# Kernel optimization log

Measured on AMD Instinct MI355X. Metric: run time of the kernel, lower is better.

Reference implementation:

```python
import jax, jax.numpy as jnp
import numpy as np
from jax import lax


def setup_inputs() -> dict:
    key = jax.random.key(0)
    ks = jax.random.split(key, 8)
    B, H, W = 1, 128, 128

    def rnd(k, shape, fan_in):
        return jax.random.normal(k, shape, dtype=jnp.float32) / np.float32(np.sqrt(fan_in))

    return {
        "x": jax.random.normal(ks[0], (B, 1, H, W), dtype=jnp.float32),
        "z": jax.random.uniform(ks[1], (B, 1), dtype=jnp.float32),
        "w_conv1": rnd(ks[2], (16, 1, 9, 9), 81),
        "b_conv1": jnp.zeros((16,), jnp.float32),
        "w_conv2": rnd(ks[3], (16, 16, 5, 5), 16 * 25),
        "b_conv2": jnp.zeros((16,), jnp.float32),
        "w_fc1": rnd(ks[4], (1024, 128), 1024),
        "b_fc1": jnp.zeros((128,), jnp.float32),
        "w_pose": rnd(ks[5], (1, 16), 1),
        "b_pose": jnp.zeros((16,), jnp.float32),
        "w_fc2": rnd(ks[6], (144, 1), 144),
        "b_fc2": jnp.zeros((1,), jnp.float32),
    }


_DN = ("NCHW", "OIHW", "NCHW")  # conv dimension numbers
_P = 32  # GQ-CNN patch size


def _maxpool2(h):
    return lax.reduce_window(h, -jnp.inf, lax.max, (1, 1, 2, 2), (1, 1, 2, 2), "VALID")


def _gqcnn(patches, z_rep, w_conv1, b_conv1, w_conv2, b_conv2,
           w_fc1, b_fc1, w_pose, b_pose, w_fc2, b_fc2):
    # patches: [N,1,32,32], z_rep: [N,1] -> quality [N,1]
    h = jax.nn.relu(lax.conv_general_dilated(patches, w_conv1, (1, 1), "SAME",
                                             dimension_numbers=_DN)
                    + b_conv1[None, :, None, None])
    h = _maxpool2(h)  # [N,16,16,16]
    h = jax.nn.relu(lax.conv_general_dilated(h, w_conv2, (1, 1), "SAME",
                                             dimension_numbers=_DN)
                    + b_conv2[None, :, None, None])
    h = _maxpool2(h)  # [N,16,8,8]
    flat = h.reshape(h.shape[0], -1)  # [N,1024]
    f = jax.nn.relu(flat @ w_fc1 + b_fc1)      # [N,128]
    p = jax.nn.relu(z_rep @ w_pose + b_pose)   # [N,16]
    return jnp.concatenate([f, p], axis=1) @ w_fc2 + b_fc2  # [N,1]


def reference(x, z, w_conv1, b_conv1, w_conv2, b_conv2,
              w_fc1, b_fc1, w_pose, b_pose, w_fc2, b_fc2):
    B, _, H, W = x.shape
    Hp, Wp = H - _P, W - _P  # loop ranges in the original: range(H-32), range(W-32)
    # Batched patch extraction replaces the O(H*W) Python loop.
    pat = lax.conv_general_dilated_patches(x, (_P, _P), (1, 1), "VALID")  # [B,1024,H-31,W-31]
    pat = pat[:, :, :Hp, :Wp]
    pat = jnp.transpose(pat, (0, 2, 3, 1)).reshape(B * Hp * Wp, 1, _P, _P)
    z_rep = jnp.repeat(z, Hp * Wp, axis=0)  # matches [B,Hp,Wp] flattening order
    q = _gqcnn(pat, z_rep, w_conv1, b_conv1, w_conv2, b_conv2,
               w_fc1, b_fc1, w_pose, b_pose, w_fc2, b_fc2)  # [N,1]
    half = _P // 2
    heat = jnp.zeros_like(x).at[:, :, half:H - half, half:W - half].set(
        q.reshape(B, 1, Hp, Wp))
    return heat
```

## Files before the change

kernel.cpp:

```cpp
#include <hip/hip_runtime.h>

typedef __attribute__((ext_vector_type(8))) short short8;
typedef __attribute__((ext_vector_type(4))) float f32x4;
typedef unsigned short u16;

__device__ __forceinline__ u16 f2bf(float f) {
    unsigned u = __builtin_bit_cast(unsigned, f);
    unsigned r = u + 0x7fffu + ((u >> 16) & 1u);
    return (u16)(r >> 16);
}

__global__ __launch_bounds__(256) void k0_prep(
    const float* __restrict__ z, const float* __restrict__ w1,
    const float* __restrict__ w2, const float* __restrict__ wfc1,
    const float* __restrict__ wpose, const float* __restrict__ bpose,
    const float* __restrict__ wfc2, const float* __restrict__ bfc2,
    float* __restrict__ out, u16* __restrict__ w1p, u16* __restrict__ w2p,
    u16* __restrict__ fc1T, float* __restrict__ cst)
{
    int gt = blockIdx.x * 256 + threadIdx.x;
    out[gt] = 0.f;

    if (gt < 2560) {
        int l = (gt >> 3) & 63, j = gt & 7, s = gt >> 9;
        int o = l & 15, bq = l >> 4;
        u16 v = 0;
        if (bq < 3) {
            int dx = bq * 4 + (j & 3);
            int dy = -1;
            if (s < 4) dy = 2 * s + (j >> 2);
            else if (j < 4) dy = 8;
            if (dy >= 0 && dx <= 8) v = f2bf(w1[o * 81 + dy * 9 + dx]);
        }
        w1p[gt] = v;
    }
    if (gt < 6656) {
        int l = (gt >> 3) & 63, j = gt & 7, s = gt >> 9;
        int o = l & 15, bq = l >> 4;
        int dy, dx, c8; bool valid = true;
        if (s < 5)       { dy = s;     dx = bq >> 1;       c8 = bq & 1; }
        else if (s < 10) { dy = s - 5; dx = 2 + (bq >> 1); c8 = bq & 1; }
        else { dy = (s - 10) + 3 * (bq & 1); dx = 4; c8 = bq >> 1; valid = (dy <= 4); }
        int ci = c8 * 8 + j;
        w2p[gt] = valid ? f2bf(w2[o * 400 + ci * 25 + dy * 5 + dx]) : (u16)0;
    }
    {
        int base = gt * 8;
        int n = base >> 10, kk = base & 1023;
        short8 v;
        #pragma unroll
        for (int j = 0; j < 8; ++j) v[j] = (short)f2bf(wfc1[(kk + j) * 128 + n]);
        *(short8*)&fc1T[base] = v;
    }
    if (gt == 0) {
        float zz = z[0];
        float s = bfc2[0];
        for (int j = 0; j < 16; ++j) {
            float p = fmaxf(zz * wpose[j] + bpose[j], 0.f);
            s += p * wfc2[128 + j];
        }
        *cst = s;
    }
}

__global__ __launch_bounds__(256, 3) void k1_feat(
    const float* __restrict__ x, const u16* __restrict__ w1p,
    const u16* __restrict__ w2p, const float* __restrict__ b1g,
    const float* __restrict__ b2g, u16* __restrict__ feat)
{
    __shared__ unsigned s2[40 * 44];
    __shared__ u16 s_h1p[20 * 20 * 24];
    __shared__ unsigned s_feat[512];

    const int tid = threadIdx.x;
    const int lane = tid & 63;
    const int wv = tid >> 6;
    const int mm = lane & 15;
    const int bq = lane >> 4;
    const int blk = blockIdx.x;
    const int py = blk / 96, px = blk % 96;

    {
        uint4 z4 = {0, 0, 0, 0};
        for (int i = tid; i < 152; i += 256) {
            int dst;
            if (i < 88) { int r8 = i / 11, c4 = i % 11;
                          int row = (r8 < 4) ? r8 : 32 + r8; dst = row * 11 + c4; }
            else        { int j = i - 88; dst = (4 + (j >> 1)) * 11 + 9 + (j & 1); }
            ((uint4*)s2)[dst] = z4;
        }
        for (int i = tid; i < 1728; i += 256) {
            int yx, d;
            if (i < 960) { int r = i / 240, off = i - r * 240;
                           int y = (r < 2) ? r : 16 + r;
                           yx = y * 20 + off / 12; d = off % 12; }
            else { int j = i - 960; int yy = 2 + j / 48; int rest = j % 48;
                   int xs = rest / 12; d = rest % 12;
                   int xx = (xs < 2) ? xs : 16 + xs; yx = yy * 20 + xx; }
            ((unsigned*)s_h1p)[yx * 12 + d] = 0;
        }
    }

    short8 w1f[5], w2f[13];
    #pragma unroll
    for (int s = 0; s < 5; ++s) w1f[s] = *(const short8*)&w1p[(s * 64 + lane) * 8];
    #pragma unroll
    for (int s = 0; s < 13; ++s) w2f[s] = *(const short8*)&w2p[(s * 64 + lane) * 8];
    const float bias1 = b1g[mm], bias2 = b2g[mm];

    for (int task = tid; task < 288; task += 256) {
        int ir = task / 9, g = task - ir * 9;
        int ic0 = g * 4 - 4;
        const float* xr = x + (py + ir) * 128 + px;
        u16 b[5];
        #pragma unroll
        for (int vi = 0; vi < 5; ++vi) {
            int ic = ic0 + vi;
            float v = (ic >= 0 && ic < 32) ? xr[ic] : 0.f;
            b[vi] = f2bf(v);
        }
        uint4 w;
        w.x = (unsigned)b[0] | ((unsigned)b[1] << 16);
        w.y = (unsigned)b[1] | ((unsigned)b[2] << 16);
        w.z = (unsigned)b[2] | ((unsigned)b[3] << 16);
        w.w = (unsigned)b[3] | ((unsigned)b[4] << 16);
        *(uint4*)&s2[(4 + ir) * 44 + g * 4] = w;
    }
    __syncthreads();

    union F { short8 s; unsigned u[4]; };
    const int dxq = (bq == 3) ? 0 : bq;

    for (int qi = 0; qi < 4; ++qi) {
        int q = wv + qi * 4;
        for (int h = 0; h < 2; ++h) {
            int pb = (2 * q) * 44 + h * 16 + mm + dxq * 4;
            unsigned u0[10], u1[10];
            #pragma unroll
            for (int i = 0; i < 10; ++i) {
                u0[i] = s2[pb + i * 44];
                u1[i] = s2[pb + i * 44 + 2];
            }
            f32x4 accA = {0, 0, 0, 0}, accB = {0, 0, 0, 0};
            #pragma unroll
            for (int s = 0; s < 5; ++s) {
                F a, b;
                a.u[0] = u0[2 * s];     a.u[1] = u1[2 * s];
                a.u[2] = u0[2 * s + 1]; a.u[3] = u1[2 * s + 1];
                int bl = (s < 4) ? 2 * s + 1 : 9;
                int bh = (s < 4) ? 2 * s + 2 : 8;
                b.u[0] = u0[bl]; b.u[1] = u1[bl];
                b.u[2] = u0[bh]; b.u[3] = u1[bh];
                accA = __builtin_amdgcn_mfma_f32_16x16x32_bf16(a.s, w1f[s], accA, 0, 0, 0);
                accB = __builtin_amdgcn_mfma_f32_16x16x32_bf16(b.s, w1f[s], accB, 0, 0, 0);
            }
            #pragma unroll
            for (int r = 0; r < 2; ++r) {
                float v = fmaxf(fmaxf(accA[2 * r], accA[2 * r + 1]),
                                fmaxf(accB[2 * r], accB[2 * r + 1]));
                v = fmaxf(v + bias1, 0.f);
                int pc = h * 8 + (bq << 1) + r;
                s_h1p[((2 + q) * 20 + (2 + pc)) * 24 + mm] = f2bf(v);
            }
        }
    }
    __syncthreads();

    for (int pi = 0; pi < 2; ++pi) {
        int q = wv + pi * 4;
        int c8s = (bq & 1) * 8;
        int baseA = ((2 * q) * 20 + mm + (bq >> 1)) * 24 + c8s;
        int baseB = baseA + 2 * 24;
        int c8C = (bq >> 1) * 8;
        int yC0 = 2 * q + 3 * (bq & 1);
        short8 A6[6], B6[6], C4[4];
        #pragma unroll
        for (int i = 0; i < 6; ++i) {
            A6[i] = *(const short8*)&s_h1p[baseA + i * 480];
            B6[i] = *(const short8*)&s_h1p[baseB + i * 480];
        }
        #pragma unroll
        for (int i = 0; i < 4; ++i) {
            int y = yC0 + i; if (y > 19) y = 19;
            C4[i] = *(const short8*)&s_h1p[(y * 20 + mm + 4) * 24 + c8C];
        }
        f32x4 accA = {0, 0, 0, 0}, accB = {0, 0, 0, 0};
        #pragma unroll
        for (int s = 0; s < 5; ++s) {
            accA = __builtin_amdgcn_mfma_f32_16x16x32_bf16(A6[s],     w2f[s], accA, 0, 0, 0);
            accB = __builtin_amdgcn_mfma_f32_16x16x32_bf16(A6[s + 1], w2f[s], accB, 0, 0, 0);
        }
        #pragma unroll
        for (int s = 0; s < 5; ++s) {
            accA = __builtin_amdgcn_mfma_f32_16x16x32_bf16(B6[s],     w2f[5 + s], accA, 0, 0, 0);
            accB = __builtin_amdgcn_mfma_f32_16x16x32_bf16(B6[s + 1], w2f[5 + s], accB, 0, 0, 0);
        }
        #pragma unroll
        for (int s = 0; s < 3; ++s) {
            accA = __builtin_amdgcn_mfma_f32_16x16x32_bf16(C4[s],     w2f[10 + s], accA, 0, 0, 0);
            accB = __builtin_amdgcn_mfma_f32_16x16x32_bf16(C4[s + 1], w2f[10 + s], accB, 0, 0, 0);
        }
        float v0, v1;
        {
            float a = fmaxf(fmaxf(accA[0], accA[1]), fmaxf(accB[0], accB[1]));
            v0 = fmaxf(a + bias2, 0.f);
            float b = fmaxf(fmaxf(accA[2], accA[3]), fmaxf(accB[2], accB[3]));
            v1 = fmaxf(b + bias2, 0.f);
        }
        unsigned dwv = (unsigned)f2bf(v0) | ((unsigned)f2bf(v1) << 16);
        s_feat[mm * 32 + ((q * 4 + bq) ^ mm)] = dwv;
    }
    __syncthreads();

    {
        int ci = tid >> 4, t = tid & 15;
        uint2 v;
        v.x = s_feat[ci * 32 + ((2 * t) ^ ci)];
        v.y = s_feat[ci * 32 + ((2 * t + 1) ^ ci)];
        *(uint2*)&feat[blk * 1024 + tid * 4] = v;
    }
}

__global__ __launch_bounds__(256) void k2_fc(
    const u16* __restrict__ feat, const u16* __restrict__ fc1T,
    const float* __restrict__ bfc1, const float* __restrict__ wfc2,
    const float* __restrict__ cst, float* __restrict__ out)
{
    __shared__ u16 sA[64 * 136];
    __shared__ u16 sB[128 * 136];
    const int tid = threadIdx.x;
    const int lane = tid & 63;
    const int wv = tid >> 6;
    const int mm = lane & 15;
    const int bq = lane >> 4;
    const int p0 = blockIdx.x * 64;

    f32x4 acc[8];
    #pragma unroll
    for (int i = 0; i < 8; ++i) acc[i] = (f32x4){0, 0, 0, 0};

    for (int kt = 0; kt < 8; ++kt) {
        for (int i = tid; i < 1024; i += 256) {
            int row = i >> 4, ch = i & 15;
            *(short8*)&sA[row * 136 + ch * 8] =
                *(const short8*)&feat[(p0 + row) * 1024 + kt * 128 + ch * 8];
        }
        for (int i = tid; i < 2048; i += 256) {
            int row = i >> 4, ch = i & 15;
            *(short8*)&sB[row * 136 + ch * 8] =
                *(const short8*)&fc1T[row * 1024 + kt * 128 + ch * 8];
        }
        __syncthreads();
        #pragma unroll
        for (int ks = 0; ks < 4; ++ks) {
            short8 aF = *(const short8*)&sA[(wv * 16 + mm) * 136 + ks * 32 + bq * 8];
            #pragma unroll
            for (int nt = 0; nt < 8; ++nt) {
                short8 bF = *(const short8*)&sB[(nt * 16 + mm) * 136 + ks * 32 + bq * 8];
                acc[nt] = __builtin_amdgcn_mfma_f32_16x16x32_bf16(aF, bF, acc[nt], 0, 0, 0);
            }
        }
        __syncthreads();
    }

    const float cpose = *cst;
    float qs[4] = {0, 0, 0, 0};
    #pragma unroll
    for (int nt = 0; nt < 8; ++nt) {
        int n = nt * 16 + mm;
        float bb = bfc1[n], wf = wfc2[n];
        #pragma unroll
        for (int r = 0; r < 4; ++r) {
            float f = fmaxf(acc[nt][r] + bb, 0.f);
            qs[r] += f * wf;
        }
    }
    #pragma unroll
    for (int r = 0; r < 4; ++r) {
        float v = qs[r];
        v += __shfl_xor(v, 1);
        v += __shfl_xor(v, 2);
        v += __shfl_xor(v, 4);
        v += __shfl_xor(v, 8);
        qs[r] = v;
    }
    if (mm == 0) {
        #pragma unroll
        for (int r = 0; r < 4; ++r) {
            int p = p0 + wv * 16 + bq * 4 + r;
            int qy = p / 96, qx = p % 96;
            out[(16 + qy) * 128 + (16 + qx)] = qs[r] + cpose;
        }
    }
}

extern "C" void kernel_launch(void* const* d_in, const int* in_sizes, int n_in,
                              void* d_out, int out_size, void* d_ws, size_t ws_size,
                              hipStream_t stream)
{
    const float* x     = (const float*)d_in[0];
    const float* z     = (const float*)d_in[1];
    const float* w1    = (const float*)d_in[2];
    const float* b1    = (const float*)d_in[3];
    const float* w2    = (const float*)d_in[4];
    const float* b2    = (const float*)d_in[5];
    const float* wfc1  = (const float*)d_in[6];
    const float* bfc1  = (const float*)d_in[7];
    const float* wpose = (const float*)d_in[8];
    const float* bpose = (const float*)d_in[9];
    const float* wfc2  = (const float*)d_in[10];
    const float* bfc2  = (const float*)d_in[11];
    float* out = (float*)d_out;

    char* ws = (char*)d_ws;
    u16*   w1p  = (u16*)(ws + 0);
    u16*   w2p  = (u16*)(ws + 8192);
    float* cst  = (float*)(ws + 22528);
    u16*   fc1T = (u16*)(ws + 24576);
    u16*   feat = (u16*)(ws + 294912);

    hipLaunchKernelGGL(k0_prep, dim3(64), dim3(256), 0, stream,
                       z, w1, w2, wfc1, wpose, bpose, wfc2, bfc2,
                       out, w1p, w2p, fc1T, cst);
    hipLaunchKernelGGL(k1_feat, dim3(9216), dim3(256), 0, stream,
                       x, w1p, w2p, b1, b2, feat);
    hipLaunchKernelGGL(k2_fc, dim3(144), dim3(256), 0, stream,
                       feat, fc1T, bfc1, wfc2, cst, out);
}
```

Before: 115.2 us.

## Use hardware bf16 pack conversion, raise conv occupancy, halve FC block tile

Replaces the software round-to-nearest bf16 conversion with the v_cvt_pk_bf16_f32 instruction in the conv kernel, packing two values per instruction. It raises the conv kernel's launch-bounds occupancy hint from 3 to 5 blocks per SM, which caps registers more tightly and risks spills given the many weight fragments held in registers. The FC kernel now uses 128-thread blocks with 32 rows each and twice as many blocks, to spread the small GEMM over more CUs. The hardware conversion may differ in NaN handling from the manual rounding, though results should match for finite inputs.

```diff
diff --git a/kernel.cpp b/kernel.cpp
--- a/kernel.cpp
+++ b/kernel.cpp
@@ -8,6 +8,11 @@
     unsigned u = __builtin_bit_cast(unsigned, f);
     unsigned r = u + 0x7fffu + ((u >> 16) & 1u);
     return (u16)(r >> 16);
+}
+__device__ __forceinline__ unsigned pkbf(float lo, float hi) {
+    unsigned r;
+    asm("v_cvt_pk_bf16_f32 %0, %1, %2" : "=v"(r) : "v"(lo), "v"(hi));
+    return r;
 }
 
 __global__ __launch_bounds__(256) void k0_prep(
@@ -63,7 +68,7 @@
     }
 }
 
-__global__ __launch_bounds__(256, 3) void k1_feat(
+__global__ __launch_bounds__(256, 5) void k1_feat(
     const float* __restrict__ x, const u16* __restrict__ w1p,
     const u16* __restrict__ w2p, const float* __restrict__ b1g,
     const float* __restrict__ b2g, u16* __restrict__ feat)
@@ -112,18 +117,17 @@
         int ir = task / 9, g = task - ir * 9;
         int ic0 = g * 4 - 4;
         const float* xr = x + (py + ir) * 128 + px;
-        u16 b[5];
+        float v[5];
         #pragma unroll
         for (int vi = 0; vi < 5; ++vi) {
             int ic = ic0 + vi;
-            float v = (ic >= 0 && ic < 32) ? xr[ic] : 0.f;
-            b[vi] = f2bf(v);
+            v[vi] = (ic >= 0 && ic < 32) ? xr[ic] : 0.f;
         }
         uint4 w;
-        w.x = (unsigned)b[0] | ((unsigned)b[1] << 16);
-        w.y = (unsigned)b[1] | ((unsigned)b[2] << 16);
-        w.z = (unsigned)b[2] | ((unsigned)b[3] << 16);
-        w.w = (unsigned)b[3] | ((unsigned)b[4] << 16);
+        w.x = pkbf(v[0], v[1]);
+        w.y = pkbf(v[1], v[2]);
+        w.z = pkbf(v[2], v[3]);
+        w.w = pkbf(v[3], v[4]);
         *(uint4*)&s2[(4 + ir) * 44 + g * 4] = w;
     }
     __syncthreads();
@@ -154,14 +158,18 @@
                 accA = __builtin_amdgcn_mfma_f32_16x16x32_bf16(a.s, w1f[s], accA, 0, 0, 0);
                 accB = __builtin_amdgcn_mfma_f32_16x16x32_bf16(b.s, w1f[s], accB, 0, 0, 0);
             }
-            #pragma unroll
-            for (int r = 0; r < 2; ++r) {
-                float v = fmaxf(fmaxf(accA[2 * r], accA[2 * r + 1]),
-                                fmaxf(accB[2 * r], accB[2 * r + 1]));
-                v = fmaxf(v + bias1, 0.f);
-                int pc = h * 8 + (bq << 1) + r;
-                s_h1p[((2 + q) * 20 + (2 + pc)) * 24 + mm] = f2bf(v);
+            float vr0, vr1;
+            {
+                float a0 = fmaxf(fmaxf(accA[0], accA[1]), fmaxf(accB[0], accB[1]));
+                vr0 = fmaxf(a0 + bias1, 0.f);
+                float a1 = fmaxf(fmaxf(accA[2], accA[3]), fmaxf(accB[2], accB[3]));
+                vr1 = fmaxf(a1 + bias1, 0.f);
             }
+            unsigned pw = pkbf(vr0, vr1);
+            int pc = h * 8 + (bq << 1);
+            int cb = ((2 + q) * 20 + (2 + pc)) * 24 + mm;
+            s_h1p[cb] = (u16)pw;
+            s_h1p[cb + 24] = (u16)(pw >> 16);
         }
     }
     __syncthreads();
@@ -207,7 +215,7 @@
             float b = fmaxf(fmaxf(accA[2], accA[3]), fmaxf(accB[2], accB[3]));
             v1 = fmaxf(b + bias2, 0.f);
         }
-        unsigned dwv = (unsigned)f2bf(v0) | ((unsigned)f2bf(v1) << 16);
+        unsigned dwv = pkbf(v0, v1);
         s_feat[mm * 32 + ((q * 4 + bq) ^ mm)] = dwv;
     }
     __syncthreads();
@@ -221,31 +229,31 @@
     }
 }
 
-__global__ __launch_bounds__(256) void k2_fc(
+__global__ __launch_bounds__(128) void k2_fc(
     const u16* __restrict__ feat, const u16* __restrict__ fc1T,
     const float* __restrict__ bfc1, const float* __restrict__ wfc2,
     const float* __restrict__ cst, float* __restrict__ out)
 {
-    __shared__ u16 sA[64 * 136];
+    __shared__ u16 sA[32 * 136];
     __shared__ u16 sB[128 * 136];
     const int tid = threadIdx.x;
     const int lane = tid & 63;
     const int wv = tid >> 6;
     const int mm = lane & 15;
     const int bq = lane >> 4;
-    const int p0 = blockIdx.x * 64;
+    const int p0 = blockIdx.x * 32;
 
     f32x4 acc[8];
     #pragma unroll
     for (int i = 0; i < 8; ++i) acc[i] = (f32x4){0, 0, 0, 0};
 
     for (int kt = 0; kt < 8; ++kt) {
-        for (int i = tid; i < 1024; i += 256) {
+        for (int i = tid; i < 512; i += 128) {
             int row = i >> 4, ch = i & 15;
             *(short8*)&sA[row * 136 + ch * 8] =
                 *(const short8*)&feat[(p0 + row) * 1024 + kt * 128 + ch * 8];
         }
-        for (int i = tid; i < 2048; i += 256) {
+        for (int i = tid; i < 2048; i += 128) {
             int row = i >> 4, ch = i & 15;
             *(short8*)&sB[row * 136 + ch * 8] =
                 *(const short8*)&fc1T[row * 1024 + kt * 128 + ch * 8];
@@ -324,6 +332,6 @@
                        out, w1p, w2p, fc1T, cst);
     hipLaunchKernelGGL(k1_feat, dim3(9216), dim3(256), 0, stream,
                        x, w1p, w2p, b1, b2, feat);
-    hipLaunchKernelGGL(k2_fc, dim3(144), dim3(256), 0, stream,
+    hipLaunchKernelGGL(k2_fc, dim3(288), dim3(128), 0, stream,
                        feat, fc1T, bfc1, wfc2, cst, out);
 }
```

Result: slower. 186.6 us (+62.0%).
